# Performance work log

Measured on AMD Instinct MI355X. Metric: run time of the kernel, lower is better.

## Reference

```python
import jax, jax.numpy as jnp
import numpy as np

CORNER_MASK = jnp.array(
    [[0, 0, 0], [0, 0, 1], [0, 1, 0], [0, 1, 1],
     [1, 0, 0], [1, 0, 1], [1, 1, 0], [1, 1, 1]], dtype=jnp.float32)


def setup_inputs() -> dict:
    key = jax.random.key(0)
    k1, k2, k3, k4 = jax.random.split(key, 4)
    DEPTH = 6
    G = 2 ** DEPTH            # 64 voxels per axis at depth 6
    C = 32                    # feature channels
    H = G * G * G             # 262144 octree nodes at depth 6
    N = 1_000_000             # query points (depth-7 node centers)

    data = jax.random.normal(k1, (1, C, H, 1), dtype=jnp.float32)
    # points scaled into [0, 2^depth]; last column is the batch id (single octree -> 0)
    xyz = jax.random.uniform(k2, (N, 3), dtype=jnp.float32) * G
    ids = jnp.zeros((N, 1), dtype=jnp.float32)
    pts = jnp.concatenate([xyz, ids], axis=1)

    # dense voxel -> node-index lookup emulating ocnn.octree_search_key;
    idx_grid = jax.random.randint(k3, (G, G, G), 0, H, dtype=jnp.int32)
    empty = jax.random.uniform(k4, (G, G, G)) < 0.1
    lut = jnp.where(empty, jnp.int32(-1), idx_grid)

    return {"data": data, "pts": pts, "lut": lut, "depth": DEPTH}


def reference(data, pts, lut, depth):
    # data: (1, C, H, 1); pts: (N, 4); lut: (G, G, G) int32; depth: python int
    G = 2 ** depth
    xyzf = pts[:, :3] - 0.5                      # (N, 3)
    xyzi = jnp.floor(xyzf)
    frac = xyzf - xyzi                           # (N, 3) fractional offsets

    corners = xyzi[:, None, :] + CORNER_MASK[None, :, :]   # (N, 8, 3)
    ci = corners.astype(jnp.int32)
    in_bounds = jnp.all((ci >= 0) & (ci < G), axis=-1)     # (N, 8)
    ci_safe = jnp.clip(ci, 0, G - 1)
    idx = lut[ci_safe[..., 0], ci_safe[..., 1], ci_safe[..., 2]]  # (N, 8)
    valid = in_bounds & (idx > -1)

    # trilinear weights: |prod((1 - mask) - frac)|, matching the torch code
    w = jnp.abs(jnp.prod((1.0 - CORNER_MASK)[None, :, :] - frac[:, None, :], axis=-1))
    w = jnp.where(valid, w, 0.0)                 # (N, 8)
    idx_safe = jnp.where(valid, idx, 0)

    feat = data[0, :, :, 0].T                    # (H, C)
    gathered = feat[idx_safe]                    # (N, 8, C)
    out = jnp.einsum('nk,nkc->nc', w, gathered)  # weighted accumulate
    norm = jnp.sum(w, axis=1, keepdims=True)     # (N, 1)
    out = out / (norm + 1e-10)
    return out.T[None, :, :, None]               # (1, C, N, 1)
```

## Files before the change

### kernel.cpp

```cpp
#include <hip/hip_runtime.h>
#include <hip/hip_fp16.h>


#define NCH 32

__global__ __launch_bounds__(256) void octri_transpose_h(
    const float* __restrict__ data, __half* __restrict__ featH, int H) {
  __shared__ float tile[32][33];
  const int h0 = blockIdx.x * 32;
  const int tx = threadIdx.x;
  const int ty = threadIdx.y;
#pragma unroll
  for (int i = 0; i < 4; ++i) {
    int c = ty + 8 * i;
    tile[c][tx] = data[(size_t)c * H + h0 + tx];
  }
  __syncthreads();
#pragma unroll
  for (int i = 0; i < 4; ++i) {
    int hl = ty + 8 * i;
    featH[(size_t)(h0 + hl) * NCH + tx] = __float2half(tile[tx][hl]);
  }
}

__global__ __launch_bounds__(256) void octri_gather_h(
    const __half* __restrict__ featH,
    const float4* __restrict__ pts4, const int* __restrict__ lut,
    const int* __restrict__ depth_p, float* __restrict__ out, int N) {
  const int t = blockIdx.x * blockDim.x + threadIdx.x;
  const int n = t >> 2;
  const int j = t & 3;
  if (n >= N) return;
  const int G = 1 << depth_p[0];

  const float4 p = pts4[n];
  const float fx = p.x - 0.5f, fy = p.y - 0.5f, fz = p.z - 0.5f;
  const float flx = floorf(fx), fly = floorf(fy), flz = floorf(fz);
  const int ix = (int)flx, iy = (int)fly, iz = (int)flz;
  const float rx = fx - flx, ry = fy - fly, rz = fz - flz;
  const float wx[2] = {1.f - rx, rx};
  const float wy[2] = {1.f - ry, ry};
  const float wz[2] = {1.f - rz, rz};

  int idx[8];
  float w[8], wsum = 0.f;
#pragma unroll
  for (int k = 0; k < 8; ++k) {
    const int bx = (k >> 2) & 1, by = (k >> 1) & 1, bz = k & 1;
    const int cx = ix + bx, cy = iy + by, cz = iz + bz;
    const bool inb = (cx >= 0) & (cx < G) & (cy >= 0) & (cy < G) &
                     (cz >= 0) & (cz < G);
    int id = -1;
    if (inb) id = lut[((size_t)cx * G + cy) * G + cz];
    const bool valid = inb && (id > -1);
    float wk = wx[bx] * wy[by] * wz[bz];
    wk = valid ? wk : 0.f;
    idx[k] = valid ? id : 0;
    w[k] = wk;
    wsum += wk;
  }

  float acc[8] = {};
#pragma unroll
  for (int k = 0; k < 8; ++k) {
    const float wk = w[k];
    const float4 hv =
        *(const float4*)(featH + (size_t)idx[k] * NCH + j * 8);
    const __half2* h2 = (const __half2*)&hv;
#pragma unroll
    for (int q = 0; q < 4; ++q) {
      const float2 f = __half22float2(h2[q]);
      acc[2 * q + 0] += wk * f.x;
      acc[2 * q + 1] += wk * f.y;
    }
  }

  const float s = 1.f / (wsum + 1e-10f);
#pragma unroll
  for (int q = 0; q < 8; ++q) {
    out[(size_t)(8 * j + q) * N + n] = acc[q] * s;
  }
}

__global__ __launch_bounds__(256) void octri_gather_direct(
    const float* __restrict__ data, const float* __restrict__ pts,
    const int* __restrict__ lut, const int* __restrict__ depth_p,
    float* __restrict__ out, int N, int H) {
  const int n = blockIdx.x * blockDim.x + threadIdx.x;
  if (n >= N) return;
  const int G = 1 << depth_p[0];

  const float4 p = ((const float4*)pts)[n];
  const float fx = p.x - 0.5f, fy = p.y - 0.5f, fz = p.z - 0.5f;
  const float flx = floorf(fx), fly = floorf(fy), flz = floorf(fz);
  const int ix = (int)flx, iy = (int)fly, iz = (int)flz;
  const float rx = fx - flx, ry = fy - fly, rz = fz - flz;
  const float wx[2] = {1.f - rx, rx};
  const float wy[2] = {1.f - ry, ry};
  const float wz[2] = {1.f - rz, rz};

  int idx[8];
  float w[8], wsum = 0.f;
#pragma unroll
  for (int k = 0; k < 8; ++k) {
    const int bx = (k >> 2) & 1, by = (k >> 1) & 1, bz = k & 1;
    const int cx = ix + bx, cy = iy + by, cz = iz + bz;
    const bool inb = (cx >= 0) & (cx < G) & (cy >= 0) & (cy < G) &
                     (cz >= 0) & (cz < G);
    int id = -1;
    if (inb) id = lut[((size_t)cx * G + cy) * G + cz];
    const bool valid = inb && (id > -1);
    float wk = wx[bx] * wy[by] * wz[bz];
    wk = valid ? wk : 0.f;
    idx[k] = valid ? id : 0;
    w[k] = wk;
    wsum += wk;
  }

  const float s = 1.f / (wsum + 1e-10f);
#pragma unroll 4
  for (int c = 0; c < NCH; ++c) {
    const float* plane = data + (size_t)c * H;
    float a = 0.f;
#pragma unroll
    for (int k = 0; k < 8; ++k) a += w[k] * plane[idx[k]];
    out[(size_t)c * N + n] = a * s;
  }
}

extern "C" void kernel_launch(void* const* d_in, const int* in_sizes, int n_in,
                              void* d_out, int out_size, void* d_ws,
                              size_t ws_size, hipStream_t stream) {
  const float* data = (const float*)d_in[0];
  const float* pts = (const float*)d_in[1];
  const int* lut = (const int*)d_in[2];
  const int* depth_p = (const int*)d_in[3];
  float* out = (float*)d_out;

  const int H = in_sizes[0] / NCH;
  const int N = in_sizes[1] / 4;

  const size_t need = (size_t)H * NCH * sizeof(__half);

  if (ws_size >= need) {
    __half* featH = (__half*)d_ws;
    dim3 tb(32, 8);
    octri_transpose_h<<<H / 32, tb, 0, stream>>>(data, featH, H);
    const int threads = 4 * N;
    octri_gather_h<<<(threads + 255) / 256, 256, 0, stream>>>(
        featH, (const float4*)pts, lut, depth_p, out, N);
  } else {
    octri_gather_direct<<<(N + 255) / 256, 256, 0, stream>>>(
        data, pts, lut, depth_p, out, N, H);
  }
}
```

Before: 275.6 us.

## Compute corner weights once per point and share via LDS in gather kernel

Before, four threads per point each recomputed the point's weights and did all eight LUT lookups. Now each thread computes the weights and indices for one point, stores them pre-normalised in shared memory, and after a barrier four lanes per point read them back to gather the fp16 features. This removes the 4x redundant LUT loads and weight math. Nontemporal loads and stores are added for the points, the input data and the output. The costs are a block-wide sync, LDS traffic and a 17 KB shared array that may reduce occupancy.

Result: no change. 274.5 us (-0.4%).

```diff
diff --git a/kernel.cpp b/kernel.cpp
--- a/kernel.cpp
+++ b/kernel.cpp
@@ -3,6 +3,8 @@
 
 
 #define NCH 32
+
+typedef float nvec4 __attribute__((ext_vector_type(4)));
 
 __global__ __launch_bounds__(256) void octri_transpose_h(
     const float* __restrict__ data, __half* __restrict__ featH, int H) {
@@ -13,7 +15,8 @@
 #pragma unroll
   for (int i = 0; i < 4; ++i) {
     int c = ty + 8 * i;
-    tile[c][tx] = data[(size_t)c * H + h0 + tx];
+    tile[c][tx] =
+        __builtin_nontemporal_load(&data[(size_t)c * H + h0 + tx]);
   }
   __syncthreads();
 #pragma unroll
@@ -23,62 +26,88 @@
   }
 }
 
-__global__ __launch_bounds__(256) void octri_gather_h(
+__global__ __launch_bounds__(256) void octri_gather2(
     const __half* __restrict__ featH,
-    const float4* __restrict__ pts4, const int* __restrict__ lut,
+    const float* __restrict__ pts, const int* __restrict__ lut,
     const int* __restrict__ depth_p, float* __restrict__ out, int N) {
-  const int t = blockIdx.x * blockDim.x + threadIdx.x;
-  const int n = t >> 2;
-  const int j = t & 3;
-  if (n >= N) return;
+  __shared__ int meta[256][17];
+
+  const int pblk = blockIdx.x * 256;
   const int G = 1 << depth_p[0];
 
-  const float4 p = pts4[n];
-  const float fx = p.x - 0.5f, fy = p.y - 0.5f, fz = p.z - 0.5f;
-  const float flx = floorf(fx), fly = floorf(fy), flz = floorf(fz);
-  const int ix = (int)flx, iy = (int)fly, iz = (int)flz;
-  const float rx = fx - flx, ry = fy - fly, rz = fz - flz;
-  const float wx[2] = {1.f - rx, rx};
-  const float wy[2] = {1.f - ry, ry};
-  const float wz[2] = {1.f - rz, rz};
+  {
+    const int p = threadIdx.x;
+    const int n = min(pblk + p, N - 1);
+    const nvec4 pt =
+        __builtin_nontemporal_load((const nvec4*)(pts + (size_t)n * 4));
+    const float fx = pt.x - 0.5f, fy = pt.y - 0.5f, fz = pt.z - 0.5f;
+    const float flx = floorf(fx), fly = floorf(fy), flz = floorf(fz);
+    const int ix = (int)flx, iy = (int)fly, iz = (int)flz;
+    const float rx = fx - flx, ry = fy - fly, rz = fz - flz;
+    const float wx[2] = {1.f - rx, rx};
+    const float wy[2] = {1.f - ry, ry};
+    const float wz[2] = {1.f - rz, rz};
+    const bool vx[2] = {(unsigned)ix < (unsigned)G,
+                        (unsigned)(ix + 1) < (unsigned)G};
+    const bool vy[2] = {(unsigned)iy < (unsigned)G,
+                        (unsigned)(iy + 1) < (unsigned)G};
+    const bool vz[2] = {(unsigned)iz < (unsigned)G,
+                        (unsigned)(iz + 1) < (unsigned)G};
 
-  int idx[8];
-  float w[8], wsum = 0.f;
+    int idx[8];
+    float w[8], wsum = 0.f;
 #pragma unroll
-  for (int k = 0; k < 8; ++k) {
-    const int bx = (k >> 2) & 1, by = (k >> 1) & 1, bz = k & 1;
-    const int cx = ix + bx, cy = iy + by, cz = iz + bz;
-    const bool inb = (cx >= 0) & (cx < G) & (cy >= 0) & (cy < G) &
-                     (cz >= 0) & (cz < G);
-    int id = -1;
-    if (inb) id = lut[((size_t)cx * G + cy) * G + cz];
-    const bool valid = inb && (id > -1);
-    float wk = wx[bx] * wy[by] * wz[bz];
-    wk = valid ? wk : 0.f;
-    idx[k] = valid ? id : 0;
-    w[k] = wk;
-    wsum += wk;
-  }
-
-  float acc[8] = {};
+    for (int k = 0; k < 8; ++k) {
+      const int bx = (k >> 2) & 1, by = (k >> 1) & 1, bz = k & 1;
+      const bool inb = vx[bx] & vy[by] & vz[bz];
+      int id = -1;
+      if (inb)
+        id = lut[((size_t)(ix + bx) * G + (iy + by)) * G + (iz + bz)];
+      const bool valid = inb && (id > -1);
+      float wk = wx[bx] * wy[by] * wz[bz];
+      wk = valid ? wk : 0.f;
+      idx[k] = valid ? id : 0;
+      w[k] = wk;
+      wsum += wk;
+    }
+    const float s = (pblk + p < N) ? (1.f / (wsum + 1e-10f)) : 0.f;
 #pragma unroll
-  for (int k = 0; k < 8; ++k) {
-    const float wk = w[k];
-    const float4 hv =
-        *(const float4*)(featH + (size_t)idx[k] * NCH + j * 8);
-    const __half2* h2 = (const __half2*)&hv;
-#pragma unroll
-    for (int q = 0; q < 4; ++q) {
-      const float2 f = __half22float2(h2[q]);
-      acc[2 * q + 0] += wk * f.x;
-      acc[2 * q + 1] += wk * f.y;
+    for (int k = 0; k < 8; ++k) {
+      meta[p][k] = idx[k];
+      meta[p][8 + k] = __float_as_int(w[k] * s);
     }
   }
+  __syncthreads();
 
-  const float s = 1.f / (wsum + 1e-10f);
+  const int lane = threadIdx.x & 63;
+  const int wid = threadIdx.x >> 6;
+  const int j = lane & 3;
 #pragma unroll
-  for (int q = 0; q < 8; ++q) {
-    out[(size_t)(8 * j + q) * N + n] = acc[q] * s;
+  for (int g = 0; g < 4; ++g) {
+    const int p = (wid << 6) + (g << 4) + (lane >> 2);
+    const int n = pblk + p;
+
+    float acc[8] = {};
+#pragma unroll
+    for (int k = 0; k < 8; ++k) {
+      const int id = meta[p][k];
+      const float ws = __int_as_float(meta[p][8 + k]);
+      const nvec4 hv = *(const nvec4*)(featH + (size_t)id * NCH + j * 8);
+      const __half2* h2 = (const __half2*)&hv;
+#pragma unroll
+      for (int q = 0; q < 4; ++q) {
+        const float2 f = __half22float2(h2[q]);
+        acc[2 * q + 0] += ws * f.x;
+        acc[2 * q + 1] += ws * f.y;
+      }
+    }
+    if (n < N) {
+#pragma unroll
+      for (int q = 0; q < 8; ++q) {
+        __builtin_nontemporal_store(acc[q],
+                                    &out[(size_t)(8 * j + q) * N + n]);
+      }
+    }
   }
 }
 
@@ -146,9 +175,9 @@
     __half* featH = (__half*)d_ws;
     dim3 tb(32, 8);
     octri_transpose_h<<<H / 32, tb, 0, stream>>>(data, featH, H);
-    const int threads = 4 * N;
-    octri_gather_h<<<(threads + 255) / 256, 256, 0, stream>>>(
-        featH, (const float4*)pts, lut, depth_p, out, N);
+    const int blocks = (N + 255) / 256;
+    octri_gather2<<<blocks, 256, 0, stream>>>(featH, pts, lut, depth_p, out,
+                                              N);
   } else {
     octri_gather_direct<<<(N + 255) / 256, 256, 0, stream>>>(
         data, pts, lut, depth_p, out, N, H);
```
